# Kernel tuning notes

Hardware: AMD Instinct MI355X
Metric: run time of the kernel (lower is better)

## Reference

```python
import jax, jax.numpy as jnp
import numpy as np

B, NB, NA, F = 4, 262144, 8192, 32

def _mk_mlp(key, d_in):
    ks = jax.random.split(key, 3)
    def lin(k, i, o):
        bound = 1.0 / np.sqrt(i)
        kw, kb = jax.random.split(k)
        w = jax.random.uniform(kw, (i, o), jnp.float32, -bound, bound)
        b = jax.random.uniform(kb, (o,), jnp.float32, -bound, bound)
        return w, b
    w1, b1 = lin(ks[0], d_in, 64)
    w2, b2 = lin(ks[1], 64, 64)
    w3, b3 = lin(ks[2], 64, 32)
    return w1, b1, w2, b2, w3, b3

def setup_inputs() -> dict:
    key = jax.random.key(0)
    ks = jax.random.split(key, 8)
    inp = {
        "bonds": jax.random.normal(ks[0], (B, NB, F), jnp.float32),
        "bond_atom_1": jax.random.randint(ks[1], (B, NB), 0, NA, jnp.int32),
        "bond_atom_2": jax.random.randint(ks[2], (B, NB), 0, NA, jnp.int32),
        "atoms": jax.random.normal(ks[3], (B, NA, F), jnp.float32),
        "state": jax.random.normal(ks[4], (B, 1, F), jnp.float32),
    }
    for name, d_in, k in (("e", 128, ks[5]), ("v", 96, ks[6]), ("u", 96, ks[7])):
        w1, b1, w2, b2, w3, b3 = _mk_mlp(k, d_in)
        inp[f"{name}_w1"], inp[f"{name}_b1"] = w1, b1
        inp[f"{name}_w2"], inp[f"{name}_b2"] = w2, b2
        inp[f"{name}_w3"], inp[f"{name}_b3"] = w3, b3
    return inp

def _mlp(x, w1, b1, w2, b2, w3, b3):
    sp = jax.nn.softplus
    h = sp(x @ w1 + b1)
    h = sp(h @ w2 + b2)
    return sp(h @ w3 + b3)

def reference(bonds, bond_atom_1, bond_atom_2, atoms, state,
              e_w1, e_b1, e_w2, e_b2, e_w3, e_b3,
              v_w1, v_b1, v_w2, v_b2, v_w3, v_b3,
              u_w1, u_b1, u_w2, u_b2, u_w3, u_b3):
    num_atoms = atoms.shape[1]
    num_bonds = bonds.shape[1]
    # gather atom features to bonds: [B, NB, F]
    a1 = jnp.take_along_axis(atoms, bond_atom_1[:, :, None], axis=1)
    a2 = jnp.take_along_axis(atoms, bond_atom_2[:, :, None], axis=1)
    st_b = jnp.broadcast_to(state, (state.shape[0], num_bonds, state.shape[2]))
    e_in = jnp.concatenate([a1, a2, bonds, st_b], axis=2)  # [B, NB, 128]
    bonds_out = _mlp(e_in, e_w1, e_b1, e_w2, e_b2, e_w3, e_b3)  # [B, NB, 32]
    # scatter-add bonds back to atoms with mean (count) normalization
    seg = jax.vmap(lambda s, i: jax.ops.segment_sum(s, i, num_segments=num_atoms))
    bonds_to_atoms = seg(bonds_out, bond_atom_1)  # [B, NA, 32]
    counts = seg(jnp.ones_like(bonds_out[..., :1]), bond_atom_1)  # [B, NA, 1]
    bonds_to_atoms = bonds_to_atoms / counts
    st_a = jnp.broadcast_to(state, (state.shape[0], num_atoms, state.shape[2]))
    v_in = jnp.concatenate([bonds_to_atoms, atoms, st_a], axis=2)  # [B, NA, 96]
    atoms_out = _mlp(v_in, v_w1, v_b1, v_w2, v_b2, v_w3, v_b3)  # [B, NA, 32]
    u_in = jnp.concatenate([
        jnp.mean(bonds_out, axis=1, keepdims=True),
        jnp.mean(atoms_out, axis=1, keepdims=True),
        state], axis=2)  # [B, 1, 96]
    state_out = _mlp(u_in, u_w1, u_b1, u_w2, u_b2, u_w3, u_b3)  # [B, 1, 32]
    return bonds_out, atoms_out, state_out
```

## Files before the change

### kernel.cpp

```cpp
#include <hip/hip_runtime.h>

#define B_   4
#define NB_  262144
#define NA_  8192
#define NB_SHIFT 18

typedef short bf16x8 __attribute__((ext_vector_type(8)));
typedef float f32x4  __attribute__((ext_vector_type(4)));

__device__ __forceinline__ float bflo(unsigned int u){ return __uint_as_float(u << 16); }
__device__ __forceinline__ float bfhi(unsigned int u){ return __uint_as_float(u & 0xffff0000u); }
__device__ __forceinline__ unsigned short f2bf(float f){
  unsigned int u = __float_as_uint(f);
  u += 0x7fffu + ((u >> 16) & 1u);
  return (unsigned short)(u >> 16);
}
__device__ __forceinline__ unsigned int packbf(float a, float b){
  unsigned int r;
  asm("v_cvt_pk_bf16_f32 %0, %1, %2" : "=v"(r) : "v"(a), "v"(b));
  return r;
}
__device__ __forceinline__ float softplus_f(float v){
  return fmaxf(v, 0.0f) + __logf(1.0f + __expf(-fabsf(v)));
}
__device__ __forceinline__ void store32f(float* dst, const float* v){
  float4* p = reinterpret_cast<float4*>(dst);
  #pragma unroll
  for (int q = 0; q < 8; ++q)
    p[q] = make_float4(v[4*q+0], v[4*q+1], v[4*q+2], v[4*q+3]);
}

__device__ __forceinline__ void stage32(unsigned int* xbuf, int tid, int r0,
                                        const float* __restrict__ src, int ncol){
  const float4* p = reinterpret_cast<const float4*>(src);
  #pragma unroll
  for (int q = 0; q < 8; ++q){
    float4 v = p[q];
    xbuf[(r0 + 2*q    )*ncol + tid] = packbf(v.x, v.y);
    xbuf[(r0 + 2*q + 1)*ncol + tid] = packbf(v.z, v.w);
  }
}

__device__ __forceinline__ void mlp_tail_packed(unsigned int* hbuf, int tid, int ncol,
                                         const float* __restrict__ W2, const float* __restrict__ B2,
                                         const float* __restrict__ W3, const float* __restrict__ B3,
                                         float* out)
{
  float acc[64];
  #pragma unroll
  for (int j = 0; j < 64; ++j) acc[j] = B2[j];
  for (int k2 = 0; k2 < 32; ++k2){
    unsigned int px = hbuf[k2*ncol + tid];
    float x0 = bflo(px), x1 = bfhi(px);
    const float* w = W2 + k2*128;
    #pragma unroll
    for (int j = 0; j < 64; ++j) acc[j] = fmaf(x0, w[j], acc[j]);
    #pragma unroll
    for (int j = 0; j < 64; ++j) acc[j] = fmaf(x1, w[64+j], acc[j]);
  }
  #pragma unroll
  for (int j2 = 0; j2 < 32; ++j2)
    hbuf[j2*ncol + tid] = packbf(softplus_f(acc[2*j2]), softplus_f(acc[2*j2+1]));

  float a3[32];
  #pragma unroll
  for (int j = 0; j < 32; ++j) a3[j] = B3[j];
  for (int k2 = 0; k2 < 32; ++k2){
    unsigned int px = hbuf[k2*ncol + tid];
    float x0 = bflo(px), x1 = bfhi(px);
    const float* w = W3 + k2*64;
    #pragma unroll
    for (int j = 0; j < 32; ++j) a3[j] = fmaf(x0, w[j], a3[j]);
    #pragma unroll
    for (int j = 0; j < 32; ++j) a3[j] = fmaf(x1, w[32+j], a3[j]);
  }
  #pragma unroll
  for (int j = 0; j < 32; ++j) out[j] = softplus_f(a3[j]);
}

struct WPtrs { const float* p[18]; };

__global__ __launch_bounds__(256) void prep_kernel(WPtrs wp, float* __restrict__ W){
  int i = blockIdx.x * 256 + threadIdx.x;
  if (i >= 39392) return;
  int idx = i;
  const int sizes[18] = {8192,64,4096,64,2048,32,
                         6144,64,4096,64,2048,32,
                         6144,64,4096,64,2048,32};
  #pragma unroll
  for (int s = 0; s < 18; ++s){
    if (idx < sizes[s]){ W[i] = wp.p[s][idx]; return; }
    idx -= sizes[s];
  }
}

__global__ __launch_bounds__(512) void biaseff_kernel(const float* __restrict__ state,
                                                      const float* __restrict__ W,
                                                      float* __restrict__ be,
                                                      float* __restrict__ bv){
  int t = threadIdx.x;
  int b = (t >> 6) & 3, j = t & 63;
  const float* st = state + b*32;
  if (t < 256){
    float a = W[8192 + j];
    #pragma unroll
    for (int k = 0; k < 32; ++k) a = fmaf(st[k], W[(96+k)*64 + j], a);
    be[b*64 + j] = a;
  } else {
    float a = W[14496 + 6144 + j];
    #pragma unroll
    for (int k = 0; k < 32; ++k) a = fmaf(st[k], W[14496 + (64+k)*64 + j], a);
    bv[b*64 + j] = a;
  }
}

__global__ __launch_bounds__(256) void swizzle_kernel(
    const float* __restrict__ ew1, const float* __restrict__ ew2,
    const float* __restrict__ ew3, unsigned short* __restrict__ Wb){
  int i = blockIdx.x*256 + threadIdx.x;
  if (i >= 14336) return;
  int j = i & 7, lane = (i >> 3) & 63;
  int quad = lane >> 4, l16 = lane & 15;
  float v;
  if (i < 8192){
    int g = i >> 9;  int nt = g & 3, kt = g >> 2;
    v = ew1[(kt*32 + quad*8 + j)*64 + nt*16 + l16];
  } else if (i < 12288){
    int g = (i - 8192) >> 9;  int nt = g & 3, kt = g >> 2;
    v = ew2[(kt*32 + quad*8 + j)*64 + nt*16 + l16];
  } else {
    int g = (i - 12288) >> 9;  int nt = g & 1, kt = g >> 1;
    v = ew3[(kt*32 + quad*8 + j)*32 + nt*16 + l16];
  }
  Wb[i] = f2bf(v);
}

__global__ __launch_bounds__(256) void hist_lds_kernel(const int* __restrict__ ba1,
                                                       int* __restrict__ partials){
  __shared__ int lh[NA_];
  const int tid = threadIdx.x;
  const int blk = blockIdx.x;
  const int b = blk >> 4;
  const size_t base = (size_t)b*NB_ + (size_t)(blk & 15)*16384;
  #pragma unroll
  for (int i = tid; i < NA_; i += 256) lh[i] = 0;
  __syncthreads();
  for (int it = 0; it < 64; ++it)
    atomicAdd(&lh[ba1[base + it*256 + tid]], 1);
  __syncthreads();
  #pragma unroll
  for (int i = tid; i < NA_; i += 256) partials[blk*NA_ + i] = lh[i];
}

__global__ __launch_bounds__(256) void reduce_kernel(const int* __restrict__ partials,
                                                     int* __restrict__ counts){
  int t = blockIdx.x*256 + threadIdx.x;
  int b = t >> 13, aa = t & (NA_-1);
  int s = 0;
  #pragma unroll
  for (int lb = 0; lb < 16; ++lb) s += partials[(b*16 + lb)*NA_ + aa];
  counts[t] = s;
}

__global__ __launch_bounds__(1024) void scan_kernel(const int* __restrict__ counts,
                                                    int* __restrict__ offsets){
  __shared__ int s[1024];
  const int tid = threadIdx.x;
  const int base = tid * 32;
  int local[32]; int sum = 0;
  #pragma unroll
  for (int i = 0; i < 32; ++i){ local[i] = counts[base + i]; sum += local[i]; }
  s[tid] = sum;
  __syncthreads();
  for (int off = 1; off < 1024; off <<= 1){
    int v = (tid >= off) ? s[tid - off] : 0;
    __syncthreads();
    s[tid] += v;
    __syncthreads();
  }
  int run = s[tid] - sum;
  #pragma unroll
  for (int i = 0; i < 32; ++i){
    offsets[base + i] = run; run += local[i];
  }
}

__global__ __launch_bounds__(256) void base_kernel(const int* __restrict__ offsets,
                                                   const int* __restrict__ partials,
                                                   int* __restrict__ bases){
  int t = blockIdx.x*256 + threadIdx.x;
  int b = t >> 13, aa = t & (NA_-1);
  int run = offsets[t];
  #pragma unroll
  for (int lb = 0; lb < 16; ++lb){
    int g = (b*16 + lb)*NA_ + aa;
    bases[g] = run; run += partials[g];
  }
}

__global__ __launch_bounds__(256) void fill_lds_kernel(const int* __restrict__ ba1,
                                                       const int* __restrict__ bases,
                                                       int* __restrict__ list){
  __shared__ int lh[NA_];
  const int tid = threadIdx.x;
  const int blk = blockIdx.x;
  const int b = blk >> 4;
  const size_t base = (size_t)b*NB_ + (size_t)(blk & 15)*16384;
  #pragma unroll
  for (int i = tid; i < NA_; i += 256) lh[i] = 0;
  __syncthreads();
  for (int it = 0; it < 64; ++it){
    int idx = it*256 + tid;
    int a = ba1[base + idx];
    int rank = atomicAdd(&lh[a], 1);
    list[bases[blk*NA_ + a] + rank] = (int)((base + idx) & (NB_ - 1));
  }
}

__global__ __launch_bounds__(256) void bonds_kernel(
    const float* __restrict__ bonds,
    const int* __restrict__ ba1,
    const int* __restrict__ ba2,
    const float* __restrict__ atoms,
    const float* __restrict__ W,
    const unsigned short* __restrict__ Wb,
    const float* __restrict__ be,
    float* __restrict__ bonds_out)
{
  __shared__ unsigned short hred[4][64*72];
  const int tid  = threadIdx.x;
  const int wave = tid >> 6, lane = tid & 63;
  const int quad = lane >> 4, l16 = lane & 15;
  const int b = blockIdx.y;
  const int rowbase = blockIdx.x*256 + wave*64;
  unsigned short* H = &hred[wave][0];

  int r[4], g1[4], g2[4];
  #pragma unroll
  for (int nt = 0; nt < 4; ++nt){
    r[nt]  = rowbase + nt*16 + l16;
    g1[nt] = ba1[(size_t)b*NB_ + r[nt]];
    g2[nt] = ba2[(size_t)b*NB_ + r[nt]];
  }

  f32x4 acc[4][4] = {};
  #pragma unroll
  for (int kt = 0; kt < 3; ++kt){
    bf16x8 wf[4];
    #pragma unroll
    for (int mt = 0; mt < 4; ++mt)
      wf[mt] = *(const bf16x8*)(Wb + ((kt*4 + mt)*64 + lane)*8);
    #pragma unroll
    for (int nt = 0; nt < 4; ++nt){
      const float* src;
      if      (kt == 0) src = atoms + ((size_t)b*NA_ + g1[nt])*32 + quad*8;
      else if (kt == 1) src = atoms + ((size_t)b*NA_ + g2[nt])*32 + quad*8;
      else              src = bonds + ((size_t)b*NB_ + r[nt])*32 + quad*8;
      float4 v0 = *(const float4*)(src);
      float4 v1 = *(const float4*)(src + 4);
      union { bf16x8 v; unsigned int u[4]; } xf;
      xf.u[0] = packbf(v0.x, v0.y);
      xf.u[1] = packbf(v0.z, v0.w);
      xf.u[2] = packbf(v1.x, v1.y);
      xf.u[3] = packbf(v1.z, v1.w);
      #pragma unroll
      for (int mt = 0; mt < 4; ++mt)
        acc[mt][nt] = __builtin_amdgcn_mfma_f32_16x16x32_bf16(wf[mt], xf.v, acc[mt][nt], 0, 0, 0);
    }
  }
  {
    const float* b1v = be + b*64;
    #pragma unroll
    for (int mt = 0; mt < 4; ++mt){
      float4 bias = *(const float4*)(b1v + mt*16 + quad*4);
      #pragma unroll
      for (int nt = 0; nt < 4; ++nt){
        unsigned int lo = packbf(softplus_f(acc[mt][nt][0] + bias.x),
                                 softplus_f(acc[mt][nt][1] + bias.y));
        unsigned int hi = packbf(softplus_f(acc[mt][nt][2] + bias.z),
                                 softplus_f(acc[mt][nt][3] + bias.w));
        *reinterpret_cast<uint2*>(H + (nt*16 + l16)*72 + mt*16 + quad*4) = make_uint2(lo, hi);
      }
    }
  }

  f32x4 acc2[4][4] = {};
  #pragma unroll
  for (int kt = 0; kt < 2; ++kt){
    bf16x8 wf[4];
    #pragma unroll
    for (int mt = 0; mt < 4; ++mt)
      wf[mt] = *(const bf16x8*)(Wb + 8192 + ((kt*4 + mt)*64 + lane)*8);
    #pragma unroll
    for (int nt = 0; nt < 4; ++nt){
      bf16x8 hf = *(const bf16x8*)(H + (nt*16 + l16)*72 + kt*32 + quad*8);
      #pragma unroll
      for (int mt = 0; mt < 4; ++mt)
        acc2[mt][nt] = __builtin_amdgcn_mfma_f32_16x16x32_bf16(wf[mt], hf, acc2[mt][nt], 0, 0, 0);
    }
  }
  {
    const float* b2v = W + 12352;
    #pragma unroll
    for (int mt = 0; mt < 4; ++mt){
      float4 bias = *(const float4*)(b2v + mt*16 + quad*4);
      #pragma unroll
      for (int nt = 0; nt < 4; ++nt){
        unsigned int lo = packbf(softplus_f(acc2[mt][nt][0] + bias.x),
                                 softplus_f(acc2[mt][nt][1] + bias.y));
        unsigned int hi = packbf(softplus_f(acc2[mt][nt][2] + bias.z),
                                 softplus_f(acc2[mt][nt][3] + bias.w));
        *reinterpret_cast<uint2*>(H + (nt*16 + l16)*72 + mt*16 + quad*4) = make_uint2(lo, hi);
      }
    }
  }

  f32x4 acc3[2][4] = {};
  #pragma unroll
  for (int kt = 0; kt < 2; ++kt){
    bf16x8 wf[2];
    #pragma unroll
    for (int mt = 0; mt < 2; ++mt)
      wf[mt] = *(const bf16x8*)(Wb + 12288 + ((kt*2 + mt)*64 + lane)*8);
    #pragma unroll
    for (int nt = 0; nt < 4; ++nt){
      bf16x8 hf = *(const bf16x8*)(H + (nt*16 + l16)*72 + kt*32 + quad*8);
      #pragma unroll
      for (int mt = 0; mt < 2; ++mt)
        acc3[mt][nt] = __builtin_amdgcn_mfma_f32_16x16x32_bf16(wf[mt], hf, acc3[mt][nt], 0, 0, 0);
    }
  }
  {
    const float* b3v = W + 14464;
    #pragma unroll
    for (int mt = 0; mt < 2; ++mt){
      float4 bias = *(const float4*)(b3v + mt*16 + quad*4);
      #pragma unroll
      for (int nt = 0; nt < 4; ++nt){
        float4 o;
        o.x = softplus_f(acc3[mt][nt][0] + bias.x);
        o.y = softplus_f(acc3[mt][nt][1] + bias.y);
        o.z = softplus_f(acc3[mt][nt][2] + bias.z);
        o.w = softplus_f(acc3[mt][nt][3] + bias.w);
        *reinterpret_cast<float4*>(bonds_out +
            ((size_t)b*NB_ + rowbase + nt*16 + l16)*32 + mt*16 + quad*4) = o;
      }
    }
  }
}

__global__ __launch_bounds__(256) void gather_kernel(
    const int* __restrict__ counts,
    const int* __restrict__ offsets,
    const int* __restrict__ list,
    const float* __restrict__ bonds_out,
    unsigned int* __restrict__ btap)
{
  int i = blockIdx.x*256 + threadIdx.x;
  int p = i & 7;
  int row = i >> 3;
  int b = row >> 13;
  int c = counts[row], o = offsets[row];
  const float* basep = bonds_out + (size_t)b*NB_*32 + p*4;
  float4 acc = make_float4(0.f, 0.f, 0.f, 0.f);
  int t = 0;
  for (; t + 2 <= c; t += 2){
    int i0 = list[o+t], i1 = list[o+t+1];
    float4 v0 = *(const float4*)(basep + (size_t)i0*32);
    float4 v1 = *(const float4*)(basep + (size_t)i1*32);
    acc.x += v0.x + v1.x; acc.y += v0.y + v1.y;
    acc.z += v0.z + v1.z; acc.w += v0.w + v1.w;
  }
  if (t < c){
    int i0 = list[o+t];
    float4 v0 = *(const float4*)(basep + (size_t)i0*32);
    acc.x += v0.x; acc.y += v0.y; acc.z += v0.z; acc.w += v0.w;
  }
  btap[(size_t)row*16 + p*2    ] = packbf(acc.x, acc.y);
  btap[(size_t)row*16 + p*2 + 1] = packbf(acc.z, acc.w);
}

__global__ __launch_bounds__(64) void atoms_kernel(
    const float* __restrict__ atoms,
    const float* __restrict__ W,
    const int* __restrict__ counts,
    const unsigned int* __restrict__ btap,
    const float* __restrict__ bv,
    float* __restrict__ atoms_out,
    float* __restrict__ bondsum,
    float* __restrict__ atomsum)
{
  __shared__ unsigned int xbuf[32*64];
  const int tid = threadIdx.x;
  const int b = blockIdx.y;
  const int row = b*NA_ + blockIdx.x*64 + tid;

  float braw[32];
  {
    const uint4* pb = reinterpret_cast<const uint4*>(btap + (size_t)row*16);
    #pragma unroll
    for (int q = 0; q < 4; ++q){
      uint4 v = pb[q];
      braw[8*q+0]=bflo(v.x); braw[8*q+1]=bfhi(v.x);
      braw[8*q+2]=bflo(v.y); braw[8*q+3]=bfhi(v.y);
      braw[8*q+4]=bflo(v.z); braw[8*q+5]=bfhi(v.z);
      braw[8*q+6]=bflo(v.w); braw[8*q+7]=bfhi(v.w);
    }
  }
  const float inv = 1.0f / (float)counts[row];
  #pragma unroll
  for (int q = 0; q < 16; ++q)
    xbuf[q*64 + tid] = packbf(braw[2*q]*inv, braw[2*q+1]*inv);
  stage32(xbuf, tid, 16, atoms + (size_t)row*32, 64);

  float acc[64];
  {
    const float* Bl = bv + b*64;
    #pragma unroll
    for (int j = 0; j < 64; ++j) acc[j] = Bl[j];
  }
  for (int k2 = 0; k2 < 32; ++k2){
    unsigned int px = xbuf[k2*64 + tid];
    float x0 = bflo(px), x1 = bfhi(px);
    const float* w = W + k2*128;
    #pragma unroll
    for (int j = 0; j < 64; ++j) acc[j] = fmaf(x0, w[j], acc[j]);
    #pragma unroll
    for (int j = 0; j < 64; ++j) acc[j] = fmaf(x1, w[64+j], acc[j]);
  }
  #pragma unroll
  for (int j2 = 0; j2 < 32; ++j2)
    xbuf[j2*64 + tid] = packbf(softplus_f(acc[2*j2]), softplus_f(acc[2*j2+1]));

  float out[32];
  mlp_tail_packed(xbuf, tid, 64, W + 6208, W + 10304, W + 10368, W + 12416, out);
  store32f(atoms_out + (size_t)row*32, out);

  #pragma unroll
  for (int f = 0; f < 32; ++f){
    float v = braw[f];
    #pragma unroll
    for (int s = 1; s < 64; s <<= 1) v += __shfl_xor(v, s);
    if (tid == 0) unsafeAtomicAdd(&bondsum[b*32 + f], v);
  }
  #pragma unroll
  for (int f = 0; f < 32; ++f){
    float v = out[f];
    #pragma unroll
    for (int s = 1; s < 64; s <<= 1) v += __shfl_xor(v, s);
    if (tid == 0) unsafeAtomicAdd(&atomsum[b*32 + f], v);
  }
}

__global__ __launch_bounds__(256) void state_kernel(
    const float* __restrict__ state,
    const float* __restrict__ W,
    const float* __restrict__ bondsum,
    const float* __restrict__ atomsum,
    float* __restrict__ state_out)
{
  __shared__ float uin[4][96];
  __shared__ float h1s[4][64];
  __shared__ float h2s[4][64];
  const int tid = threadIdx.x;
  const int b = tid >> 6;
  const int j = tid & 63;
  if (j < 32){
    uin[b][j]      = bondsum[b*32 + j] * (1.0f/(float)NB_);
    uin[b][32 + j] = atomsum[b*32 + j] * (1.0f/(float)NA_);
    uin[b][64 + j] = state[(size_t)b*32 + j];
  }
  __syncthreads();
  float a1 = W[6144 + j];
  for (int k = 0; k < 96; ++k) a1 = fmaf(uin[b][k], W[k*64 + j], a1);
  h1s[b][j] = softplus_f(a1);
  __syncthreads();
  float a2 = W[10304 + j];
  for (int k = 0; k < 64; ++k) a2 = fmaf(h1s[b][k], W[6208 + k*64 + j], a2);
  h2s[b][j] = softplus_f(a2);
  __syncthreads();
  if (j < 32){
    float a3 = W[12416 + j];
    for (int k = 0; k < 64; ++k) a3 = fmaf(h2s[b][k], W[10368 + k*32 + j], a3);
    state_out[b*32 + j] = softplus_f(a3);
  }
}

extern "C" void kernel_launch(void* const* d_in, const int* in_sizes, int n_in,
                              void* d_out, int out_size, void* d_ws, size_t ws_size,
                              hipStream_t stream)
{
  (void)in_sizes; (void)n_in; (void)out_size; (void)ws_size;
  const float* bonds = (const float*)d_in[0];
  const int*   ba1   = (const int*)d_in[1];
  const int*   ba2   = (const int*)d_in[2];
  const float* atoms = (const float*)d_in[3];
  const float* state = (const float*)d_in[4];

  int*          counts  = (int*)d_ws;
  int*          offsets = counts + 32768;
  int*          list    = counts + 98304;
  unsigned int* btap    = (unsigned int*)d_ws + 1146880;
  float*        bondsum = (float*)d_ws + 1671168;
  float*        atomsum = (float*)d_ws + 1671296;
  float*        W       = (float*)d_ws + 1671424;
  unsigned short* Wb    = (unsigned short*)((unsigned int*)d_ws + 1710816);
  float*        be      = (float*)d_ws + 1717984;
  float*        bv      = (float*)d_ws + 1718240;

  int* partials = list;
  int* bases    = (int*)btap;

  hipMemsetAsync(bondsum, 0, 256 * sizeof(float), stream);

  WPtrs wp;
  for (int s = 0; s < 18; ++s) wp.p[s] = (const float*)d_in[5 + s];
  prep_kernel<<<154, 256, 0, stream>>>(wp, W);
  biaseff_kernel<<<1, 512, 0, stream>>>(state, W, be, bv);
  swizzle_kernel<<<56, 256, 0, stream>>>((const float*)d_in[5], (const float*)d_in[7],
                                         (const float*)d_in[9], Wb);

  hist_lds_kernel<<<64, 256, 0, stream>>>(ba1, partials);
  reduce_kernel<<<128, 256, 0, stream>>>(partials, counts);
  scan_kernel<<<1, 1024, 0, stream>>>(counts, offsets);
  base_kernel<<<128, 256, 0, stream>>>(offsets, partials, bases);
  fill_lds_kernel<<<64, 256, 0, stream>>>(ba1, bases, list);

  float* out_bonds = (float*)d_out;
  float* out_atoms = out_bonds + (size_t)B_*NB_*32;
  float* out_state = out_atoms + (size_t)B_*NA_*32;

  bonds_kernel<<<dim3(NB_/256, B_), 256, 0, stream>>>(bonds, ba1, ba2, atoms,
                                                      W, Wb, be, out_bonds);
  gather_kernel<<<(B_*NA_*8)/256, 256, 0, stream>>>(counts, offsets, list, out_bonds, btap);
  atoms_kernel<<<dim3(NA_/64, B_), 64, 0, stream>>>(atoms, W + 14496,
                                                    counts, btap, bv, out_atoms,
                                                    bondsum, atomsum);
  state_kernel<<<1, 256, 0, stream>>>(state, W + 26944, bondsum, atomsum, out_state);
}
```

Measured before the change: 613.3 us.

## Move atom MLP to MFMA and restructure bond MLP per row-tile

The scalar-FMA atom MLP is replaced by a bf16 MFMA version with swizzled v-weights, 256-thread blocks, and per-wave partial sums in place of full 64-lane shuffle reductions. The mean normalization moves into the gather kernel, which changes the bf16 rounding point. The bond MLP now processes one 16-row tile at a time with a small LDS scratch and occupancy hint, cutting register pressure at some loss of weight-fragment reuse. The histogram and fill kernels switch to 1024-thread blocks.

```diff
diff --git a/kernel.cpp b/kernel.cpp
--- a/kernel.cpp
+++ b/kernel.cpp
@@ -23,59 +23,10 @@
 __device__ __forceinline__ float softplus_f(float v){
   return fmaxf(v, 0.0f) + __logf(1.0f + __expf(-fabsf(v)));
 }
-__device__ __forceinline__ void store32f(float* dst, const float* v){
-  float4* p = reinterpret_cast<float4*>(dst);
-  #pragma unroll
-  for (int q = 0; q < 8; ++q)
-    p[q] = make_float4(v[4*q+0], v[4*q+1], v[4*q+2], v[4*q+3]);
-}
-
-__device__ __forceinline__ void stage32(unsigned int* xbuf, int tid, int r0,
-                                        const float* __restrict__ src, int ncol){
-  const float4* p = reinterpret_cast<const float4*>(src);
-  #pragma unroll
-  for (int q = 0; q < 8; ++q){
-    float4 v = p[q];
-    xbuf[(r0 + 2*q    )*ncol + tid] = packbf(v.x, v.y);
-    xbuf[(r0 + 2*q + 1)*ncol + tid] = packbf(v.z, v.w);
-  }
-}
-
-__device__ __forceinline__ void mlp_tail_packed(unsigned int* hbuf, int tid, int ncol,
-                                         const float* __restrict__ W2, const float* __restrict__ B2,
-                                         const float* __restrict__ W3, const float* __restrict__ B3,
-                                         float* out)
-{
-  float acc[64];
-  #pragma unroll
-  for (int j = 0; j < 64; ++j) acc[j] = B2[j];
-  for (int k2 = 0; k2 < 32; ++k2){
-    unsigned int px = hbuf[k2*ncol + tid];
-    float x0 = bflo(px), x1 = bfhi(px);
-    const float* w = W2 + k2*128;
-    #pragma unroll
-    for (int j = 0; j < 64; ++j) acc[j] = fmaf(x0, w[j], acc[j]);
-    #pragma unroll
-    for (int j = 0; j < 64; ++j) acc[j] = fmaf(x1, w[64+j], acc[j]);
-  }
-  #pragma unroll
-  for (int j2 = 0; j2 < 32; ++j2)
-    hbuf[j2*ncol + tid] = packbf(softplus_f(acc[2*j2]), softplus_f(acc[2*j2+1]));
-
-  float a3[32];
-  #pragma unroll
-  for (int j = 0; j < 32; ++j) a3[j] = B3[j];
-  for (int k2 = 0; k2 < 32; ++k2){
-    unsigned int px = hbuf[k2*ncol + tid];
-    float x0 = bflo(px), x1 = bfhi(px);
-    const float* w = W3 + k2*64;
-    #pragma unroll
-    for (int j = 0; j < 32; ++j) a3[j] = fmaf(x0, w[j], a3[j]);
-    #pragma unroll
-    for (int j = 0; j < 32; ++j) a3[j] = fmaf(x1, w[32+j], a3[j]);
-  }
-  #pragma unroll
-  for (int j = 0; j < 32; ++j) out[j] = softplus_f(a3[j]);
+__device__ __forceinline__ void lds_fence(){
+  asm volatile("" ::: "memory");
+  __builtin_amdgcn_wave_barrier();
+  __builtin_amdgcn_sched_barrier(0);
 }
 
 struct WPtrs { const float* p[18]; };
@@ -116,40 +67,60 @@
 
 __global__ __launch_bounds__(256) void swizzle_kernel(
     const float* __restrict__ ew1, const float* __restrict__ ew2,
-    const float* __restrict__ ew3, unsigned short* __restrict__ Wb){
+    const float* __restrict__ ew3,
+    const float* __restrict__ vw1, const float* __restrict__ vw2,
+    const float* __restrict__ vw3,
+    unsigned short* __restrict__ Wb, unsigned short* __restrict__ Wbv){
   int i = blockIdx.x*256 + threadIdx.x;
-  if (i >= 14336) return;
+  if (i >= 24576) return;
   int j = i & 7, lane = (i >> 3) & 63;
   int quad = lane >> 4, l16 = lane & 15;
+  int krow = quad*8 + j;
   float v;
-  if (i < 8192){
-    int g = i >> 9;  int nt = g & 3, kt = g >> 2;
-    v = ew1[(kt*32 + quad*8 + j)*64 + nt*16 + l16];
-  } else if (i < 12288){
-    int g = (i - 8192) >> 9;  int nt = g & 3, kt = g >> 2;
-    v = ew2[(kt*32 + quad*8 + j)*64 + nt*16 + l16];
+  if (i < 14336){
+    if (i < 8192){
+      int g = i >> 9;  int mt = g & 3, kt = g >> 2;
+      v = ew1[(kt*32 + krow)*64 + mt*16 + l16];
+    } else if (i < 12288){
+      int g = (i - 8192) >> 9;  int mt = g & 3, kt = g >> 2;
+      v = ew2[(kt*32 + krow)*64 + mt*16 + l16];
+    } else {
+      int g = (i - 12288) >> 9;  int mt = g & 1, kt = g >> 1;
+      v = ew3[(kt*32 + krow)*32 + mt*16 + l16];
+    }
+    Wb[i] = f2bf(v);
   } else {
-    int g = (i - 12288) >> 9;  int nt = g & 1, kt = g >> 1;
-    v = ew3[(kt*32 + quad*8 + j)*32 + nt*16 + l16];
-  }
-  Wb[i] = f2bf(v);
-}
-
-__global__ __launch_bounds__(256) void hist_lds_kernel(const int* __restrict__ ba1,
-                                                       int* __restrict__ partials){
+    int o = i - 14336;
+    if (o < 4096){
+      int g = o >> 9;  int mt = g & 3, kt = g >> 2;
+      v = vw1[(kt*32 + krow)*64 + mt*16 + l16];
+    } else if (o < 8192){
+      int g = (o - 4096) >> 9;  int mt = g & 3, kt = g >> 2;
+      v = vw2[(kt*32 + krow)*64 + mt*16 + l16];
+    } else {
+      int g = (o - 8192) >> 9;  int mt = g & 1, kt = g >> 1;
+      v = vw3[(kt*32 + krow)*32 + mt*16 + l16];
+    }
+    Wbv[o] = f2bf(v);
+  }
+}
+
+__global__ __launch_bounds__(1024) void hist_lds_kernel(const int* __restrict__ ba1,
+                                                        int* __restrict__ partials){
   __shared__ int lh[NA_];
   const int tid = threadIdx.x;
   const int blk = blockIdx.x;
   const int b = blk >> 4;
   const size_t base = (size_t)b*NB_ + (size_t)(blk & 15)*16384;
   #pragma unroll
-  for (int i = tid; i < NA_; i += 256) lh[i] = 0;
-  __syncthreads();
-  for (int it = 0; it < 64; ++it)
-    atomicAdd(&lh[ba1[base + it*256 + tid]], 1);
-  __syncthreads();
-  #pragma unroll
-  for (int i = tid; i < NA_; i += 256) partials[blk*NA_ + i] = lh[i];
+  for (int i = tid; i < NA_; i += 1024) lh[i] = 0;
+  __syncthreads();
+  #pragma unroll
+  for (int it = 0; it < 16; ++it)
+    atomicAdd(&lh[ba1[base + it*1024 + tid]], 1);
+  __syncthreads();
+  #pragma unroll
+  for (int i = tid; i < NA_; i += 1024) partials[blk*NA_ + i] = lh[i];
 }
 
 __global__ __launch_bounds__(256) void reduce_kernel(const int* __restrict__ partials,
@@ -198,26 +169,27 @@
   }
 }
 
-__global__ __launch_bounds__(256) void fill_lds_kernel(const int* __restrict__ ba1,
-                                                       const int* __restrict__ bases,
-                                                       int* __restrict__ list){
+__global__ __launch_bounds__(1024) void fill_lds_kernel(const int* __restrict__ ba1,
+                                                        const int* __restrict__ bases,
+                                                        int* __restrict__ list){
   __shared__ int lh[NA_];
   const int tid = threadIdx.x;
   const int blk = blockIdx.x;
   const int b = blk >> 4;
   const size_t base = (size_t)b*NB_ + (size_t)(blk & 15)*16384;
   #pragma unroll
-  for (int i = tid; i < NA_; i += 256) lh[i] = 0;
-  __syncthreads();
-  for (int it = 0; it < 64; ++it){
-    int idx = it*256 + tid;
+  for (int i = tid; i < NA_; i += 1024) lh[i] = 0;
+  __syncthreads();
+  #pragma unroll
+  for (int it = 0; it < 16; ++it){
+    int idx = it*1024 + tid;
     int a = ba1[base + idx];
     int rank = atomicAdd(&lh[a], 1);
     list[bases[blk*NA_ + a] + rank] = (int)((base + idx) & (NB_ - 1));
   }
 }
 
-__global__ __launch_bounds__(256) void bonds_kernel(
+__global__ __launch_bounds__(256, 5) void bonds_kernel(
     const float* __restrict__ bonds,
     const int* __restrict__ ba1,
     const int* __restrict__ ba2,
@@ -227,13 +199,13 @@
     const float* __restrict__ be,
     float* __restrict__ bonds_out)
 {
-  __shared__ unsigned short hred[4][64*72];
+  __shared__ unsigned short hsall[4][1160];
   const int tid  = threadIdx.x;
   const int wave = tid >> 6, lane = tid & 63;
   const int quad = lane >> 4, l16 = lane & 15;
   const int b = blockIdx.y;
   const int rowbase = blockIdx.x*256 + wave*64;
-  unsigned short* H = &hred[wave][0];
+  unsigned short* hwr = &hsall[wave][0] + l16*72;
 
   int r[4], g1[4], g2[4];
   #pragma unroll
@@ -243,15 +215,11 @@
     g2[nt] = ba2[(size_t)b*NB_ + r[nt]];
   }
 
-  f32x4 acc[4][4] = {};
-  #pragma unroll
-  for (int kt = 0; kt < 3; ++kt){
-    bf16x8 wf[4];
-    #pragma unroll
-    for (int mt = 0; mt < 4; ++mt)
-      wf[mt] = *(const bf16x8*)(Wb + ((kt*4 + mt)*64 + lane)*8);
-    #pragma unroll
-    for (int nt = 0; nt < 4; ++nt){
+  #pragma unroll
+  for (int nt = 0; nt < 4; ++nt){
+    f32x4 a1[4] = {};
+    #pragma unroll
+    for (int kt = 0; kt < 3; ++kt){
       const float* src;
       if      (kt == 0) src = atoms + ((size_t)b*NA_ + g1[nt])*32 + quad*8;
       else if (kt == 1) src = atoms + ((size_t)b*NA_ + g2[nt])*32 + quad*8;
@@ -264,87 +232,60 @@
       xf.u[2] = packbf(v1.x, v1.y);
       xf.u[3] = packbf(v1.z, v1.w);
       #pragma unroll
-      for (int mt = 0; mt < 4; ++mt)
-        acc[mt][nt] = __builtin_amdgcn_mfma_f32_16x16x32_bf16(wf[mt], xf.v, acc[mt][nt], 0, 0, 0);
-    }
-  }
-  {
-    const float* b1v = be + b*64;
+      for (int mt = 0; mt < 4; ++mt){
+        bf16x8 wf = *(const bf16x8*)(Wb + ((kt*4 + mt)*64 + lane)*8);
+        a1[mt] = __builtin_amdgcn_mfma_f32_16x16x32_bf16(wf, xf.v, a1[mt], 0, 0, 0);
+      }
+    }
+    lds_fence();
     #pragma unroll
     for (int mt = 0; mt < 4; ++mt){
-      float4 bias = *(const float4*)(b1v + mt*16 + quad*4);
-      #pragma unroll
-      for (int nt = 0; nt < 4; ++nt){
-        unsigned int lo = packbf(softplus_f(acc[mt][nt][0] + bias.x),
-                                 softplus_f(acc[mt][nt][1] + bias.y));
-        unsigned int hi = packbf(softplus_f(acc[mt][nt][2] + bias.z),
-                                 softplus_f(acc[mt][nt][3] + bias.w));
-        *reinterpret_cast<uint2*>(H + (nt*16 + l16)*72 + mt*16 + quad*4) = make_uint2(lo, hi);
-      }
-    }
-  }
-
-  f32x4 acc2[4][4] = {};
-  #pragma unroll
-  for (int kt = 0; kt < 2; ++kt){
-    bf16x8 wf[4];
-    #pragma unroll
-    for (int mt = 0; mt < 4; ++mt)
-      wf[mt] = *(const bf16x8*)(Wb + 8192 + ((kt*4 + mt)*64 + lane)*8);
-    #pragma unroll
-    for (int nt = 0; nt < 4; ++nt){
-      bf16x8 hf = *(const bf16x8*)(H + (nt*16 + l16)*72 + kt*32 + quad*8);
-      #pragma unroll
-      for (int mt = 0; mt < 4; ++mt)
-        acc2[mt][nt] = __builtin_amdgcn_mfma_f32_16x16x32_bf16(wf[mt], hf, acc2[mt][nt], 0, 0, 0);
-    }
-  }
-  {
-    const float* b2v = W + 12352;
+      float4 bias = *(const float4*)(be + b*64 + mt*16 + quad*4);
+      unsigned int lo = packbf(softplus_f(a1[mt][0] + bias.x), softplus_f(a1[mt][1] + bias.y));
+      unsigned int hi = packbf(softplus_f(a1[mt][2] + bias.z), softplus_f(a1[mt][3] + bias.w));
+      *reinterpret_cast<uint2*>(hwr + mt*16 + quad*4) = make_uint2(lo, hi);
+    }
+    lds_fence();
+
+    f32x4 a2[4] = {};
+    #pragma unroll
+    for (int kt = 0; kt < 2; ++kt){
+      bf16x8 hf = *(const bf16x8*)(hwr + kt*32 + quad*8);
+      #pragma unroll
+      for (int mt = 0; mt < 4; ++mt){
+        bf16x8 wf = *(const bf16x8*)(Wb + 8192 + ((kt*4 + mt)*64 + lane)*8);
+        a2[mt] = __builtin_amdgcn_mfma_f32_16x16x32_bf16(wf, hf, a2[mt], 0, 0, 0);
+      }
+    }
+    lds_fence();
     #pragma unroll
     for (int mt = 0; mt < 4; ++mt){
-      float4 bias = *(const float4*)(b2v + mt*16 + quad*4);
-      #pragma unroll
-      for (int nt = 0; nt < 4; ++nt){
-        unsigned int lo = packbf(softplus_f(acc2[mt][nt][0] + bias.x),
-                                 softplus_f(acc2[mt][nt][1] + bias.y));
-        unsigned int hi = packbf(softplus_f(acc2[mt][nt][2] + bias.z),
-                                 softplus_f(acc2[mt][nt][3] + bias.w));
-        *reinterpret_cast<uint2*>(H + (nt*16 + l16)*72 + mt*16 + quad*4) = make_uint2(lo, hi);
-      }
-    }
-  }
-
-  f32x4 acc3[2][4] = {};
-  #pragma unroll
-  for (int kt = 0; kt < 2; ++kt){
-    bf16x8 wf[2];
-    #pragma unroll
-    for (int mt = 0; mt < 2; ++mt)
-      wf[mt] = *(const bf16x8*)(Wb + 12288 + ((kt*2 + mt)*64 + lane)*8);
-    #pragma unroll
-    for (int nt = 0; nt < 4; ++nt){
-      bf16x8 hf = *(const bf16x8*)(H + (nt*16 + l16)*72 + kt*32 + quad*8);
-      #pragma unroll
-      for (int mt = 0; mt < 2; ++mt)
-        acc3[mt][nt] = __builtin_amdgcn_mfma_f32_16x16x32_bf16(wf[mt], hf, acc3[mt][nt], 0, 0, 0);
-    }
-  }
-  {
-    const float* b3v = W + 14464;
+      float4 bias = *(const float4*)(W + 12352 + mt*16 + quad*4);
+      unsigned int lo = packbf(softplus_f(a2[mt][0] + bias.x), softplus_f(a2[mt][1] + bias.y));
+      unsigned int hi = packbf(softplus_f(a2[mt][2] + bias.z), softplus_f(a2[mt][3] + bias.w));
+      *reinterpret_cast<uint2*>(hwr + mt*16 + quad*4) = make_uint2(lo, hi);
+    }
+    lds_fence();
+
+    f32x4 a3[2] = {};
+    #pragma unroll
+    for (int kt = 0; kt < 2; ++kt){
+      bf16x8 hf = *(const bf16x8*)(hwr + kt*32 + quad*8);
+      #pragma unroll
+      for (int mt = 0; mt < 2; ++mt){
+        bf16x8 wf = *(const bf16x8*)(Wb + 12288 + ((kt*2 + mt)*64 + lane)*8);
+        a3[mt] = __builtin_amdgcn_mfma_f32_16x16x32_bf16(wf, hf, a3[mt], 0, 0, 0);
+      }
+    }
     #pragma unroll
     for (int mt = 0; mt < 2; ++mt){
-      float4 bias = *(const float4*)(b3v + mt*16 + quad*4);
-      #pragma unroll
-      for (int nt = 0; nt < 4; ++nt){
-        float4 o;
-        o.x = softplus_f(acc3[mt][nt][0] + bias.x);
-        o.y = softplus_f(acc3[mt][nt][1] + bias.y);
-        o.z = softplus_f(acc3[mt][nt][2] + bias.z);
-        o.w = softplus_f(acc3[mt][nt][3] + bias.w);
-        *reinterpret_cast<float4*>(bonds_out +
-            ((size_t)b*NB_ + rowbase + nt*16 + l16)*32 + mt*16 + quad*4) = o;
-      }
+      float4 bias = *(const float4*)(W + 14464 + mt*16 + quad*4);
+      float4 o;
+      o.x = softplus_f(a3[mt][0] + bias.x);
+      o.y = softplus_f(a3[mt][1] + bias.y);
+      o.z = softplus_f(a3[mt][2] + bias.z);
+      o.w = softplus_f(a3[mt][3] + bias.w);
+      *reinterpret_cast<float4*>(bonds_out + ((size_t)b*NB_ + r[nt])*32 + mt*16 + quad*4) = o;
     }
   }
 }
@@ -376,79 +317,135 @@
     float4 v0 = *(const float4*)(basep + (size_t)i0*32);
     acc.x += v0.x; acc.y += v0.y; acc.z += v0.z; acc.w += v0.w;
   }
-  btap[(size_t)row*16 + p*2    ] = packbf(acc.x, acc.y);
-  btap[(size_t)row*16 + p*2 + 1] = packbf(acc.z, acc.w);
-}
-
-__global__ __launch_bounds__(64) void atoms_kernel(
+  float inv = 1.0f / (float)c;
+  btap[(size_t)row*16 + p*2    ] = packbf(acc.x*inv, acc.y*inv);
+  btap[(size_t)row*16 + p*2 + 1] = packbf(acc.z*inv, acc.w*inv);
+}
+
+__global__ __launch_bounds__(256, 5) void atoms_kernel(
     const float* __restrict__ atoms,
-    const float* __restrict__ W,
+    const float* __restrict__ Wv,
     const int* __restrict__ counts,
     const unsigned int* __restrict__ btap,
     const float* __restrict__ bv,
+    const unsigned short* __restrict__ Wbv,
     float* __restrict__ atoms_out,
     float* __restrict__ bondsum,
     float* __restrict__ atomsum)
 {
-  __shared__ unsigned int xbuf[32*64];
-  const int tid = threadIdx.x;
+  __shared__ unsigned short hsall[4][1160];
+  const int tid  = threadIdx.x;
+  const int wave = tid >> 6, lane = tid & 63;
+  const int quad = lane >> 4, l16 = lane & 15;
   const int b = blockIdx.y;
-  const int row = b*NA_ + blockIdx.x*64 + tid;
-
-  float braw[32];
-  {
-    const uint4* pb = reinterpret_cast<const uint4*>(btap + (size_t)row*16);
-    #pragma unroll
-    for (int q = 0; q < 4; ++q){
-      uint4 v = pb[q];
-      braw[8*q+0]=bflo(v.x); braw[8*q+1]=bfhi(v.x);
-      braw[8*q+2]=bflo(v.y); braw[8*q+3]=bfhi(v.y);
-      braw[8*q+4]=bflo(v.z); braw[8*q+5]=bfhi(v.z);
-      braw[8*q+6]=bflo(v.w); braw[8*q+7]=bfhi(v.w);
-    }
-  }
-  const float inv = 1.0f / (float)counts[row];
-  #pragma unroll
-  for (int q = 0; q < 16; ++q)
-    xbuf[q*64 + tid] = packbf(braw[2*q]*inv, braw[2*q+1]*inv);
-  stage32(xbuf, tid, 16, atoms + (size_t)row*32, 64);
-
-  float acc[64];
-  {
-    const float* Bl = bv + b*64;
-    #pragma unroll
-    for (int j = 0; j < 64; ++j) acc[j] = Bl[j];
-  }
-  for (int k2 = 0; k2 < 32; ++k2){
-    unsigned int px = xbuf[k2*64 + tid];
-    float x0 = bflo(px), x1 = bfhi(px);
-    const float* w = W + k2*128;
-    #pragma unroll
-    for (int j = 0; j < 64; ++j) acc[j] = fmaf(x0, w[j], acc[j]);
-    #pragma unroll
-    for (int j = 0; j < 64; ++j) acc[j] = fmaf(x1, w[64+j], acc[j]);
-  }
-  #pragma unroll
-  for (int j2 = 0; j2 < 32; ++j2)
-    xbuf[j2*64 + tid] = packbf(softplus_f(acc[2*j2]), softplus_f(acc[2*j2+1]));
-
-  float out[32];
-  mlp_tail_packed(xbuf, tid, 64, W + 6208, W + 10304, W + 10368, W + 12416, out);
-  store32f(atoms_out + (size_t)row*32, out);
-
-  #pragma unroll
-  for (int f = 0; f < 32; ++f){
-    float v = braw[f];
-    #pragma unroll
-    for (int s = 1; s < 64; s <<= 1) v += __shfl_xor(v, s);
-    if (tid == 0) unsafeAtomicAdd(&bondsum[b*32 + f], v);
-  }
-  #pragma unroll
-  for (int f = 0; f < 32; ++f){
-    float v = out[f];
-    #pragma unroll
-    for (int s = 1; s < 64; s <<= 1) v += __shfl_xor(v, s);
-    if (tid == 0) unsafeAtomicAdd(&atomsum[b*32 + f], v);
+  const int arowbase = blockIdx.x*256 + wave*64;
+  unsigned short* hwr = &hsall[wave][0] + l16*72;
+
+  int arow[4], cnt[4];
+  #pragma unroll
+  for (int nt = 0; nt < 4; ++nt){
+    arow[nt] = b*NA_ + arowbase + nt*16 + l16;
+    cnt[nt]  = counts[arow[nt]];
+  }
+
+  float p1[8] = {0,0,0,0,0,0,0,0};
+  float p2[8] = {0,0,0,0,0,0,0,0};
+
+  #pragma unroll
+  for (int nt = 0; nt < 4; ++nt){
+    f32x4 a1[4] = {};
+    {
+      union { uint4 q; bf16x8 v; } bt;
+      bt.q = *(const uint4*)(btap + (size_t)arow[nt]*16 + quad*4);
+      float cf = (float)cnt[nt];
+      p1[0] += bflo(bt.q.x)*cf; p1[1] += bfhi(bt.q.x)*cf;
+      p1[2] += bflo(bt.q.y)*cf; p1[3] += bfhi(bt.q.y)*cf;
+      p1[4] += bflo(bt.q.z)*cf; p1[5] += bfhi(bt.q.z)*cf;
+      p1[6] += bflo(bt.q.w)*cf; p1[7] += bfhi(bt.q.w)*cf;
+      #pragma unroll
+      for (int mt = 0; mt < 4; ++mt){
+        bf16x8 wf = *(const bf16x8*)(Wbv + ((0*4 + mt)*64 + lane)*8);
+        a1[mt] = __builtin_amdgcn_mfma_f32_16x16x32_bf16(wf, bt.v, a1[mt], 0, 0, 0);
+      }
+    }
+    {
+      const float* src = atoms + (size_t)arow[nt]*32 + quad*8;
+      float4 v0 = *(const float4*)(src);
+      float4 v1 = *(const float4*)(src + 4);
+      union { bf16x8 v; unsigned int u[4]; } xf;
+      xf.u[0] = packbf(v0.x, v0.y);
+      xf.u[1] = packbf(v0.z, v0.w);
+      xf.u[2] = packbf(v1.x, v1.y);
+      xf.u[3] = packbf(v1.z, v1.w);
+      #pragma unroll
+      for (int mt = 0; mt < 4; ++mt){
+        bf16x8 wf = *(const bf16x8*)(Wbv + ((1*4 + mt)*64 + lane)*8);
+        a1[mt] = __builtin_amdgcn_mfma_f32_16x16x32_bf16(wf, xf.v, a1[mt], 0, 0, 0);
+      }
+    }
+    lds_fence();
+    #pragma unroll
+    for (int mt = 0; mt < 4; ++mt){
+      float4 bias = *(const float4*)(bv + b*64 + mt*16 + quad*4);
+      unsigned int lo = packbf(softplus_f(a1[mt][0] + bias.x), softplus_f(a1[mt][1] + bias.y));
+      unsigned int hi = packbf(softplus_f(a1[mt][2] + bias.z), softplus_f(a1[mt][3] + bias.w));
+      *reinterpret_cast<uint2*>(hwr + mt*16 + quad*4) = make_uint2(lo, hi);
+    }
+    lds_fence();
+
+    f32x4 a2[4] = {};
+    #pragma unroll
+    for (int kt = 0; kt < 2; ++kt){
+      bf16x8 hf = *(const bf16x8*)(hwr + kt*32 + quad*8);
+      #pragma unroll
+      for (int mt = 0; mt < 4; ++mt){
+        bf16x8 wf = *(const bf16x8*)(Wbv + 4096 + ((kt*4 + mt)*64 + lane)*8);
+        a2[mt] = __builtin_amdgcn_mfma_f32_16x16x32_bf16(wf, hf, a2[mt], 0, 0, 0);
+      }
+    }
+    lds_fence();
+    #pragma unroll
+    for (int mt = 0; mt < 4; ++mt){
+      float4 bias = *(const float4*)(Wv + 10304 + mt*16 + quad*4);
+      unsigned int lo = packbf(softplus_f(a2[mt][0] + bias.x), softplus_f(a2[mt][1] + bias.y));
+      unsigned int hi = packbf(softplus_f(a2[mt][2] + bias.z), softplus_f(a2[mt][3] + bias.w));
+      *reinterpret_cast<uint2*>(hwr + mt*16 + quad*4) = make_uint2(lo, hi);
+    }
+    lds_fence();
+
+    f32x4 a3[2] = {};
+    #pragma unroll
+    for (int kt = 0; kt < 2; ++kt){
+      bf16x8 hf = *(const bf16x8*)(hwr + kt*32 + quad*8);
+      #pragma unroll
+      for (int mt = 0; mt < 2; ++mt){
+        bf16x8 wf = *(const bf16x8*)(Wbv + 8192 + ((kt*2 + mt)*64 + lane)*8);
+        a3[mt] = __builtin_amdgcn_mfma_f32_16x16x32_bf16(wf, hf, a3[mt], 0, 0, 0);
+      }
+    }
+    #pragma unroll
+    for (int mt = 0; mt < 2; ++mt){
+      float4 bias = *(const float4*)(Wv + 12416 + mt*16 + quad*4);
+      float4 o;
+      o.x = softplus_f(a3[mt][0] + bias.x);
+      o.y = softplus_f(a3[mt][1] + bias.y);
+      o.z = softplus_f(a3[mt][2] + bias.z);
+      o.w = softplus_f(a3[mt][3] + bias.w);
+      p2[mt*4+0] += o.x; p2[mt*4+1] += o.y; p2[mt*4+2] += o.z; p2[mt*4+3] += o.w;
+      *reinterpret_cast<float4*>(atoms_out + (size_t)arow[nt]*32 + mt*16 + quad*4) = o;
+    }
+  }
+
+  #pragma unroll
+  for (int j = 0; j < 8; ++j){
+    float v = p1[j];
+    v += __shfl_xor(v, 1); v += __shfl_xor(v, 2);
+    v += __shfl_xor(v, 4); v += __shfl_xor(v, 8);
+    if (l16 == 0) unsafeAtomicAdd(&bondsum[b*32 + quad*8 + j], v);
+    float w = p2[j];
+    w += __shfl_xor(w, 1); w += __shfl_xor(w, 2);
+    w += __shfl_xor(w, 4); w += __shfl_xor(w, 8);
+    if (l16 == 0) unsafeAtomicAdd(&atomsum[b*32 + (j>>2)*16 + quad*4 + (j&3)], w);
   }
 }
 
@@ -499,6 +496,7 @@
 
   int*          counts  = (int*)d_ws;
   int*          offsets = counts + 32768;
+  unsigned short* Wbv   = (unsigned short*)((unsigned int*)d_ws + 65536);
   int*          list    = counts + 98304;
   unsigned int* btap    = (unsigned int*)d_ws + 1146880;
   float*        bondsum = (float*)d_ws + 1671168;
@@ -517,14 +515,16 @@
   for (int s = 0; s < 18; ++s) wp.p[s] = (const float*)d_in[5 + s];
   prep_kernel<<<154, 256, 0, stream>>>(wp, W);
   biaseff_kernel<<<1, 512, 0, stream>>>(state, W, be, bv);
-  swizzle_kernel<<<56, 256, 0, stream>>>((const float*)d_in[5], (const float*)d_in[7],
-                                         (const float*)d_in[9], Wb);
-
-  hist_lds_kernel<<<64, 256, 0, stream>>>(ba1, partials);
+  swizzle_kernel<<<96, 256, 0, stream>>>((const float*)d_in[5], (const float*)d_in[7],
+                                         (const float*)d_in[9],
+                                         (const float*)d_in[11], (const float*)d_in[13],
+                                         (const float*)d_in[15], Wb, Wbv);
+
+  hist_lds_kernel<<<64, 1024, 0, stream>>>(ba1, partials);
   reduce_kernel<<<128, 256, 0, stream>>>(partials, counts);
   scan_kernel<<<1, 1024, 0, stream>>>(counts, offsets);
   base_kernel<<<128, 256, 0, stream>>>(offsets, partials, bases);
-  fill_lds_kernel<<<64, 256, 0, stream>>>(ba1, bases, list);
+  fill_lds_kernel<<<64, 1024, 0, stream>>>(ba1, bases, list);
 
   float* out_bonds = (float*)d_out;
   float* out_atoms = out_bonds + (size_t)B_*NB_*32;
@@ -533,8 +533,8 @@
   bonds_kernel<<<dim3(NB_/256, B_), 256, 0, stream>>>(bonds, ba1, ba2, atoms,
                                                       W, Wb, be, out_bonds);
   gather_kernel<<<(B_*NA_*8)/256, 256, 0, stream>>>(counts, offsets, list, out_bonds, btap);
-  atoms_kernel<<<dim3(NA_/64, B_), 64, 0, stream>>>(atoms, W + 14496,
-                                                    counts, btap, bv, out_atoms,
-                                                    bondsum, atomsum);
+  atoms_kernel<<<dim3(NA_/256, B_), 256, 0, stream>>>(atoms, W + 14496,
+                                                      counts, btap, bv, Wbv, out_atoms,
+                                                      bondsum, atomsum);
   state_kernel<<<1, 256, 0, stream>>>(state, W + 26944, bondsum, atomsum, out_state);
 }
```

Result: faster. 542.7 us (-11.5%).
